# Kernel optimization log

Measured on AMD Instinct MI355X. Metric: run time of the kernel, lower is better.

Reference implementation:

```python
import jax, jax.numpy as jnp
import numpy as np

V, NB, NJ, NP, NK = 6890, 10, 24, 207, 19
PARENTS = np.array([-1, 0, 0, 0, 1, 2, 3, 4, 5, 6, 7, 8, 9, 9, 9, 12, 13, 14, 16, 17, 18, 19, 20, 21])


def setup_inputs():
    key = jax.random.key(0)
    ks = jax.random.split(key, 9)
    B = 1024
    beta = jax.random.normal(ks[0], (B, NB), jnp.float32)
    theta = jax.random.normal(ks[1], (B, NJ * 3), jnp.float32) * 0.3  # axis-angle per joint
    trans = jax.random.normal(ks[2], (B, 3), jnp.float32)
    v_template = jax.random.normal(ks[3], (V, 3), jnp.float32)
    shapedirs = jax.random.normal(ks[4], (NB, V * 3), jnp.float32) * 0.03
    Jr = jax.random.uniform(ks[5], (V, NJ), jnp.float32)
    J_regressor = Jr / jnp.sum(Jr, axis=0, keepdims=True)
    posedirs = jax.random.normal(ks[6], (NP, V * 3), jnp.float32) * 0.01
    jr = jax.random.uniform(ks[7], (V, NK), jnp.float32)
    joint_regressor = jr / jnp.sum(jr, axis=0, keepdims=True)
    w = jax.random.uniform(ks[8], (V, NJ), jnp.float32)
    weights = w / jnp.sum(w, axis=1, keepdims=True)  # LBS weights, rows sum to 1
    return dict(beta=beta, theta=theta, trans=trans, v_template=v_template,
                shapedirs=shapedirs, J_regressor=J_regressor, posedirs=posedirs,
                joint_regressor=joint_regressor, weights=weights)


def batch_rodrigues(theta):
    # theta: (N,3) axis-angle -> (N,3,3) rotation matrices via quaternions (HMR-style)
    angle = jnp.linalg.norm(theta + 1e-8, axis=1, keepdims=True)
    half = angle * 0.5
    v = (theta / angle) * jnp.sin(half)
    quat = jnp.concatenate([jnp.cos(half), v], axis=1)
    quat = quat / jnp.linalg.norm(quat, axis=1, keepdims=True)
    w, x, y, z = quat[:, 0], quat[:, 1], quat[:, 2], quat[:, 3]
    rot = jnp.stack([
        1 - 2 * (y * y + z * z), 2 * (x * y - w * z), 2 * (x * z + w * y),
        2 * (x * y + w * z), 1 - 2 * (x * x + z * z), 2 * (y * z - w * x),
        2 * (x * z - w * y), 2 * (y * z + w * x), 1 - 2 * (x * x + y * y)], axis=1)
    return rot.reshape(-1, 3, 3)


def batch_global_rigid_transformation(Rs, J):
    # Rs: (B,24,3,3), J: (B,24,3); rotate_base=True
    B = Rs.shape[0]
    rot_x = jnp.array([[1., 0., 0.], [0., -1., 0.], [0., 0., -1.]], jnp.float32)
    root_R = Rs[:, 0] @ rot_x

    def make_A(R, t):  # (B,3,3),(B,3) -> (B,4,4)
        top = jnp.concatenate([R, t[:, :, None]], axis=2)
        bot = jnp.broadcast_to(jnp.array([0., 0., 0., 1.], jnp.float32), (B, 1, 4))
        return jnp.concatenate([top, bot], axis=1)

    results = [make_A(root_R, J[:, 0])]
    for i in range(1, NJ):  # fixed 24-joint kinematic chain
        t = J[:, i] - J[:, PARENTS[i]]
        results.append(results[PARENTS[i]] @ make_A(Rs[:, i], t))
    res = jnp.stack(results, axis=1)  # (B,24,4,4)
    new_J = res[:, :, :3, 3]
    j_w0 = jnp.concatenate([J, jnp.zeros_like(J[:, :, :1])], axis=2)  # (B,24,4), homo w=0
    init_bone = jnp.einsum('bjrc,bjc->bjr', res, j_w0)
    A = res.at[:, :, :, 3].add(-init_bone)  # subtract only last column (matches F.pad trick)
    return new_J, A


def reference(beta, theta, trans, v_template, shapedirs, J_regressor, posedirs, joint_regressor, weights):
    B = beta.shape[0]
    v_shaped = (beta @ shapedirs).reshape(B, V, 3) + v_template
    J = jnp.einsum('bvc,vj->bjc', v_shaped, J_regressor)  # (B,24,3)
    Rs = batch_rodrigues(theta.reshape(-1, 3)).reshape(B, NJ, 3, 3)
    pose_feature = (Rs[:, 1:] - jnp.eye(3, dtype=Rs.dtype)).reshape(B, NP)
    v_posed = (pose_feature @ posedirs).reshape(B, V, 3) + v_shaped
    _, A = batch_global_rigid_transformation(Rs, J)
    T = jnp.einsum('vj,bjrc->bvrc', weights, A)  # (B,V,4,4) per-vertex skinning transforms
    homo = jnp.concatenate([v_posed, jnp.ones((B, V, 1), v_posed.dtype)], axis=2)
    verts = jnp.einsum('bvrc,bvc->bvr', T, homo)[:, :, :3] + trans[:, None, :]
    joints = jnp.einsum('bvc,vk->bkc', verts, joint_regressor)  # (B,19,3)
    return joints
```

## Files before the change

kernel.cpp:

```cpp
#include <hip/hip_runtime.h>
#include <hip/hip_bf16.h>

constexpr int Vn   = 6890;
constexpr int VC3  = 20670;
constexpr int NKB  = 216;
constexpr int QT   = 224;
constexpr int NMG  = 14;
constexpr int NCOL = 480;
constexpr int WR   = 1440;
constexpr int MC   = 1368;
constexpr int KSEG = 12;
constexpr int KCH  = 18;
constexpr int RB   = 158;

using bf16x8  = __attribute__((ext_vector_type(8))) short;
using floatx4 = __attribute__((ext_vector_type(4))) float;

__device__ __forceinline__ unsigned short f2bf(float f) {
    unsigned int u = __float_as_uint(f);
    unsigned int r = (u + 0x7FFFu + ((u >> 16) & 1u)) >> 16;
    return (unsigned short)r;
}

__global__ __launch_bounds__(256) void k0_build(
    const float* __restrict__ vt, const float* __restrict__ sdirs,
    const float* __restrict__ pdirs, const float* __restrict__ Jreg,
    const float* __restrict__ jreg, const float* __restrict__ wts,
    unsigned short* __restrict__ Af, unsigned short* __restrict__ Bf,
    float* __restrict__ Jacc)
{
    int bx = blockIdx.x, t = threadIdx.x;
    if (bx < 756) {
        int mg = bx / 54, ub = bx % 54;
        int ql = t & 15, q = mg * 16 + ql;
        int uu = ub * 16 + (t >> 4);
        int v0 = uu * 8, base = 3 * v0;
        float buf[24];
        if (q == 0) {
            #pragma unroll
            for (int i = 0; i < 24; ++i) buf[i] = (v0 + i / 3 < Vn) ? 1.f : 0.f;
        } else {
            const float* src = nullptr;
            if (q == 1) src = vt;
            else if (q >= 2 && q < 12)   src = sdirs + (size_t)(q - 2) * VC3;
            else if (q >= 12 && q < 219) src = pdirs + (size_t)(q - 12) * VC3;
            if (src && base + 23 < VC3) {
                #pragma unroll
                for (int i = 0; i < 12; ++i) {
                    float2 f = *(const float2*)(src + base + 2 * i);
                    buf[2 * i] = f.x; buf[2 * i + 1] = f.y;
                }
            } else {
                #pragma unroll
                for (int i = 0; i < 24; ++i)
                    buf[i] = (src && base + i < VC3) ? src[base + i] : 0.f;
            }
        }
        int kb = uu >> 2, quad = uu & 3;
        size_t foff = (size_t)(ql + quad * 16) * 8;
        #pragma unroll
        for (int c = 0; c < 3; ++c) {
            bf16x8 o;
            #pragma unroll
            for (int j = 0; j < 8; ++j) o[j] = (short)f2bf(buf[3 * j + c]);
            *(bf16x8*)(Af + ((size_t)(c * NMG + mg) * NKB + kb) * 512 + foff) = o;
        }
        return;
    }
    bx -= 756;
    if (bx < 108) {
        int v0 = bx * 64;
        __shared__ float js[64 * 19], wsh[64 * 24], Jsh[64 * 24];
        for (int i = t; i < 64 * 19; i += 256)
            js[i] = (v0 * 19 + i < Vn * 19) ? jreg[v0 * 19 + i] : 0.f;
        for (int i = t; i < 64 * 24; i += 256) {
            wsh[i] = (v0 * 24 + i < Vn * 24) ? wts[v0 * 24 + i] : 0.f;
            Jsh[i] = (v0 * 24 + i < Vn * 24) ? Jreg[v0 * 24 + i] : 0.f;
        }
        __syncthreads();
        for (int s = t; s < 4096; s += 256) {
            int clow = s & 15, w = s >> 4;
            int vg = w & 7, chigh = w >> 3;
            int col = chigh * 16 + clow;
            int kb = (v0 >> 5) + (vg >> 2);
            bf16x8 o;
            #pragma unroll
            for (int j = 0; j < 8; ++j) {
                int vl = vg * 8 + j;
                float val = 0.f;
                if (col < 456)      val = js[vl * 19 + col / 24] * wsh[vl * 24 + col % 24];
                else if (col < 480) val = Jsh[vl * 24 + (col - 456)];
                o[j] = (short)f2bf(val);
            }
            *(bf16x8*)(Bf + ((size_t)chigh * NKB + kb) * 512
                          + (size_t)(clow + (vg & 3) * 16) * 8) = o;
        }
        return;
    }
    for (int i = t; i < 792; i += 256) Jacc[i] = 0.f;
}

__device__ __forceinline__ void k1_load(bf16x8 (&a)[2], bf16x8 (&b)[4],
    const unsigned short* __restrict__ ap, const unsigned short* __restrict__ bp, int i)
{
    a[0] = *(const bf16x8*)(ap + (size_t)(0 * NKB + i) * 512);
    a[1] = *(const bf16x8*)(ap + (size_t)(1 * NKB + i) * 512);
    b[0] = *(const bf16x8*)(bp + (size_t)(0 * NKB + i) * 512);
    b[1] = *(const bf16x8*)(bp + (size_t)(1 * NKB + i) * 512);
    b[2] = *(const bf16x8*)(bp + (size_t)(2 * NKB + i) * 512);
    b[3] = *(const bf16x8*)(bp + (size_t)(3 * NKB + i) * 512);
}

__global__ __launch_bounds__(64) void k1_mfma(
    const unsigned short* __restrict__ Af, const unsigned short* __restrict__ Bf,
    float* __restrict__ P, float* __restrict__ Jacc)
{
    int l = threadIdx.x;
    int bid = blockIdx.x;
    int wid = (bid & 7) * 252 + (bid >> 3);
    int kseg = wid / 168; int r = wid % 168;
    int c = r / 56; r %= 56;
    int mt = r >> 3, nt = r & 7;
    int kb0 = kseg * KCH;

    const unsigned short* ap = Af + ((size_t)(c * NMG + mt * 2) * NKB + kb0) * 512 + l * 8;
    const unsigned short* bp = Bf + ((size_t)(nt * 4) * NKB + kb0) * 512 + l * 8;

    floatx4 acc[2][4];
    #pragma unroll
    for (int mi = 0; mi < 2; ++mi)
        #pragma unroll
        for (int ni = 0; ni < 4; ++ni) acc[mi][ni] = floatx4{0.f, 0.f, 0.f, 0.f};

    bf16x8 a[3][2], b[3][4];
    k1_load(a[0], b[0], ap, bp, 0);
    k1_load(a[1], b[1], ap, bp, 1);
    #pragma unroll
    for (int i = 0; i < KCH; ++i) {
        if (i + 2 < KCH) k1_load(a[(i + 2) % 3], b[(i + 2) % 3], ap, bp, i + 2);
        bf16x8 (&ac)[2] = a[i % 3];
        bf16x8 (&bc)[4] = b[i % 3];
        #pragma unroll
        for (int mi = 0; mi < 2; ++mi)
            #pragma unroll
            for (int ni = 0; ni < 4; ++ni)
                acc[mi][ni] = __builtin_amdgcn_mfma_f32_16x16x32_bf16(ac[mi], bc[ni], acc[mi][ni], 0, 0, 0);
    }
    float* Ps = P + (size_t)kseg * WR * QT;
    int lr = l & 15, rq = (l >> 4) * 4;
    #pragma unroll
    for (int mi = 0; mi < 2; ++mi)
        #pragma unroll
        for (int ni = 0; ni < 4; ++ni) {
            int col = nt * 64 + ni * 16 + lr;
            if (col < NCOL) {
                int q0 = mt * 32 + mi * 16 + rq;
                *(floatx4*)(Ps + (size_t)(col * 3 + c) * QT + q0) = acc[mi][ni];
            }
        }
    if (mt == 0 && nt == 7 && rq < 12) {
        #pragma unroll
        for (int ni = 0; ni < 2; ++ni) {
            int col = 448 + ni * 16 + lr;
            if (col >= 456 && col < 480) {
                #pragma unroll
                for (int rr = 0; rr < 4; ++rr) {
                    int q = rq + rr;
                    if (q >= 1 && q < 12)
                        atomicAdd(&Jacc[(size_t)((col - 456) * 3 + c) * 11 + (q - 1)],
                                  acc[0][ni][rr]);
                }
            }
        }
    }
}

__global__ __launch_bounds__(256) void k12_reduce_prep(
    const float* __restrict__ P, const float* __restrict__ Jacc,
    const float* __restrict__ beta, const float* __restrict__ theta,
    unsigned short* __restrict__ Wb3, float* __restrict__ w1g,
    unsigned short* __restrict__ xbf, float* __restrict__ RAg, float* __restrict__ tAg)
{
    int t = threadIdx.x;
    if (blockIdx.x < RB) {
        int g = blockIdx.x * 256 + t;
        if (g >= WR * 28) return;
        int colc = g / 28, q0 = (g % 28) * 8;
        float v[8] = {0, 0, 0, 0, 0, 0, 0, 0};
        #pragma unroll
        for (int s = 0; s < KSEG; ++s) {
            const float4* p = (const float4*)(P + ((size_t)s * WR + colc) * QT + q0);
            float4 x0 = p[0], x1 = p[1];
            v[0] += x0.x; v[1] += x0.y; v[2] += x0.z; v[3] += x0.w;
            v[4] += x1.x; v[5] += x1.y; v[6] += x1.z; v[7] += x1.w;
        }
        if (colc < 1408) {
            bf16x8 o;
            #pragma unroll
            for (int j = 0; j < 8; ++j)
                o[j] = (short)((colc < MC) ? f2bf(v[j]) : 0);
            *(bf16x8*)(Wb3 + ((size_t)(colc >> 4) * 7 + (q0 >> 5)) * 512
                           + (size_t)((colc & 15) + ((q0 >> 3) & 3) * 16) * 8) = o;
        }
        if (q0 == 0 && colc % 3 == 0 && colc < MC) w1g[colc / 3] = v[0];
        return;
    }
    int b = blockIdx.x - RB;
    __shared__ float Rs[24][9];
    __shared__ float Jl[24][3];
    __shared__ float resR[24][9];
    __shared__ float rest[24][3];
    __shared__ float bet[10];

    if (t < 10) bet[t] = beta[b * 10 + t];
    if (t < 24) {
        float t0 = theta[b * 72 + t * 3 + 0];
        float t1 = theta[b * 72 + t * 3 + 1];
        float t2 = theta[b * 72 + t * 3 + 2];
        float e0 = t0 + 1e-8f, e1 = t1 + 1e-8f, e2 = t2 + 1e-8f;
        float angle = sqrtf(e0 * e0 + e1 * e1 + e2 * e2);
        float half = 0.5f * angle;
        float sh = sinf(half), ch = cosf(half);
        float s = sh / angle;
        float qx = t0 * s, qy = t1 * s, qz = t2 * s;
        float qn = sqrtf(ch * ch + qx * qx + qy * qy + qz * qz);
        float w = ch / qn, x = qx / qn, y = qy / qn, z = qz / qn;
        Rs[t][0] = 1.f - 2.f * (y * y + z * z);
        Rs[t][1] = 2.f * (x * y - w * z);
        Rs[t][2] = 2.f * (x * z + w * y);
        Rs[t][3] = 2.f * (x * y + w * z);
        Rs[t][4] = 1.f - 2.f * (x * x + z * z);
        Rs[t][5] = 2.f * (y * z - w * x);
        Rs[t][6] = 2.f * (x * z - w * y);
        Rs[t][7] = 2.f * (y * z + w * x);
        Rs[t][8] = 1.f - 2.f * (x * x + y * y);
    }
    __syncthreads();
    if (t < 72) {
        const float* basep = Jacc + (size_t)t * 11;
        float acc = basep[0];
        #pragma unroll
        for (int n = 0; n < 10; ++n) acc += bet[n] * basep[1 + n];
        Jl[t / 3][t % 3] = acc;
    }
    for (int q = t; q < QT; q += 256) {
        float xv = 0.f;
        if (q == 1) xv = 1.f;
        else if (q >= 2 && q < 12) xv = bet[q - 2];
        else if (q >= 12 && q < 219) {
            int p = q - 12;
            int jj = 1 + p / 9, e = p % 9;
            float rr = Rs[jj][e];
            if (e == 0 || e == 4 || e == 8) rr -= 1.f;
            xv = rr;
        }
        xbf[((size_t)(b >> 4) * 7 + (q >> 5)) * 512
            + (size_t)((b & 15) + ((q >> 3) & 3) * 16) * 8 + (q & 7)] = f2bf(xv);
    }
    __syncthreads();
    if (t == 0) {
        const int par[24] = {-1,0,0,0,1,2,3,4,5,6,7,8,9,9,9,12,13,14,16,17,18,19,20,21};
        #pragma unroll
        for (int rr = 0; rr < 3; ++rr) {
            resR[0][rr * 3 + 0] =  Rs[0][rr * 3 + 0];
            resR[0][rr * 3 + 1] = -Rs[0][rr * 3 + 1];
            resR[0][rr * 3 + 2] = -Rs[0][rr * 3 + 2];
            rest[0][rr] = Jl[0][rr];
        }
        for (int i = 1; i < 24; ++i) {
            int p = par[i];
            float t0 = Jl[i][0] - Jl[p][0];
            float t1 = Jl[i][1] - Jl[p][1];
            float t2 = Jl[i][2] - Jl[p][2];
            #pragma unroll
            for (int rr = 0; rr < 3; ++rr) {
                float a0 = resR[p][rr * 3 + 0], a1 = resR[p][rr * 3 + 1], a2 = resR[p][rr * 3 + 2];
                resR[i][rr * 3 + 0] = a0 * Rs[i][0] + a1 * Rs[i][3] + a2 * Rs[i][6];
                resR[i][rr * 3 + 1] = a0 * Rs[i][1] + a1 * Rs[i][4] + a2 * Rs[i][7];
                resR[i][rr * 3 + 2] = a0 * Rs[i][2] + a1 * Rs[i][5] + a2 * Rs[i][8];
                rest[i][rr] = a0 * t0 + a1 * t1 + a2 * t2 + rest[p][rr];
            }
        }
    }
    __syncthreads();
    if (t < 216) RAg[(size_t)b * 216 + t] = resR[t / 9][t % 9];
    if (t < 72) {
        int j = t / 3, c = t % 3;
        tAg[(size_t)b * 72 + t] = rest[j][c]
            - (resR[j][c * 3 + 0] * Jl[j][0] + resR[j][c * 3 + 1] * Jl[j][1]
             + resR[j][c * 3 + 2] * Jl[j][2]);
    }
}

__global__ __launch_bounds__(256) void k3_mfma(
    const unsigned short* __restrict__ Wb3, const unsigned short* __restrict__ xbf,
    float* __restrict__ Mg)
{
    int w = threadIdx.x >> 6, l = threadIdx.x & 63;
    int wm = w & 1, wn = w >> 1;
    int ct = blockIdx.x % 22, bt = blockIdx.x / 22;
    int mg0 = ct * 4 + wm * 2;
    int bg0 = bt * 8 + wn * 4;
    const unsigned short* ap = Wb3 + (size_t)mg0 * 7 * 512 + l * 8;
    const unsigned short* bp = xbf + (size_t)bg0 * 7 * 512 + l * 8;

    floatx4 acc[2][4];
    #pragma unroll
    for (int mi = 0; mi < 2; ++mi)
        #pragma unroll
        for (int ni = 0; ni < 4; ++ni) acc[mi][ni] = floatx4{0.f, 0.f, 0.f, 0.f};

    #pragma unroll
    for (int kk = 0; kk < 7; ++kk) {
        bf16x8 a0 = *(const bf16x8*)(ap + (size_t)(0 * 7 + kk) * 512);
        bf16x8 a1 = *(const bf16x8*)(ap + (size_t)(1 * 7 + kk) * 512);
        bf16x8 b0 = *(const bf16x8*)(bp + (size_t)(0 * 7 + kk) * 512);
        bf16x8 b1 = *(const bf16x8*)(bp + (size_t)(1 * 7 + kk) * 512);
        bf16x8 b2 = *(const bf16x8*)(bp + (size_t)(2 * 7 + kk) * 512);
        bf16x8 b3 = *(const bf16x8*)(bp + (size_t)(3 * 7 + kk) * 512);
        acc[0][0] = __builtin_amdgcn_mfma_f32_16x16x32_bf16(a0, b0, acc[0][0], 0, 0, 0);
        acc[0][1] = __builtin_amdgcn_mfma_f32_16x16x32_bf16(a0, b1, acc[0][1], 0, 0, 0);
        acc[0][2] = __builtin_amdgcn_mfma_f32_16x16x32_bf16(a0, b2, acc[0][2], 0, 0, 0);
        acc[0][3] = __builtin_amdgcn_mfma_f32_16x16x32_bf16(a0, b3, acc[0][3], 0, 0, 0);
        acc[1][0] = __builtin_amdgcn_mfma_f32_16x16x32_bf16(a1, b0, acc[1][0], 0, 0, 0);
        acc[1][1] = __builtin_amdgcn_mfma_f32_16x16x32_bf16(a1, b1, acc[1][1], 0, 0, 0);
        acc[1][2] = __builtin_amdgcn_mfma_f32_16x16x32_bf16(a1, b2, acc[1][2], 0, 0, 0);
        acc[1][3] = __builtin_amdgcn_mfma_f32_16x16x32_bf16(a1, b3, acc[1][3], 0, 0, 0);
    }
    int lr = l & 15, rq = (l >> 4) * 4;
    #pragma unroll
    for (int mi = 0; mi < 2; ++mi)
        #pragma unroll
        for (int ni = 0; ni < 4; ++ni) {
            int b  = bt * 128 + wn * 64 + ni * 16 + lr;
            int cc = (mg0 + mi) * 16 + rq;
            if (cc < MC)
                *(floatx4*)(Mg + (size_t)b * MC + cc) = acc[mi][ni];
        }
}

__global__ __launch_bounds__(256) void k4_combine(
    const float* __restrict__ Mg, const float* __restrict__ RAg,
    const float* __restrict__ tAg, const float* __restrict__ w1g,
    const float* __restrict__ trans, float* __restrict__ out)
{
    __shared__ float w1s[456];
    __shared__ float Ms[4 * MC];
    __shared__ float RAs[4 * 216];
    __shared__ float tAs[4 * 72];
    int tid = threadIdx.x;
    int b0 = blockIdx.x * 4;
    for (int i = tid; i < 456; i += 256) w1s[i] = w1g[i];
    for (int i = tid; i < 4 * MC; i += 256) Ms[i] = Mg[(size_t)b0 * MC + i];
    for (int i = tid; i < 4 * 216; i += 256) RAs[i] = RAg[(size_t)b0 * 216 + i];
    for (int i = tid; i < 4 * 72; i += 256) tAs[i] = tAg[(size_t)b0 * 72 + i];
    __syncthreads();
    if (tid < 228) {
        int lb = tid / 57, kc = tid % 57;
        int k = kc / 3, c = kc % 3;
        int b = b0 + lb;
        float acc = trans[b * 3 + c];
        const float* Mrow = Ms + lb * MC;
        const float* RAr  = RAs + lb * 216;
        const float* tAr  = tAs + lb * 72;
        #pragma unroll
        for (int j = 0; j < 24; ++j) {
            int kj = k * 24 + j;
            float m0 = Mrow[kj * 3 + 0], m1 = Mrow[kj * 3 + 1], m2 = Mrow[kj * 3 + 2];
            acc += RAr[j * 9 + c * 3 + 0] * m0
                 + RAr[j * 9 + c * 3 + 1] * m1
                 + RAr[j * 9 + c * 3 + 2] * m2
                 + tAr[j * 3 + c] * w1s[kj];
        }
        out[b * 57 + kc] = acc;
    }
}

extern "C" void kernel_launch(void* const* d_in, const int* in_sizes, int n_in,
                              void* d_out, int out_size, void* d_ws, size_t ws_size,
                              hipStream_t stream)
{
    const float* beta  = (const float*)d_in[0];
    const float* theta = (const float*)d_in[1];
    const float* trans = (const float*)d_in[2];
    const float* vt    = (const float*)d_in[3];
    const float* sdirs = (const float*)d_in[4];
    const float* Jreg  = (const float*)d_in[5];
    const float* pdirs = (const float*)d_in[6];
    const float* jreg  = (const float*)d_in[7];
    const float* wts   = (const float*)d_in[8];
    float* out = (float*)d_out;
    int B = in_sizes[0] / 10;

    unsigned short* Af  = (unsigned short*)d_ws;
    unsigned short* Bf  = Af + (size_t)42 * NKB * 512;
    unsigned short* Wb3 = Bf + (size_t)32 * NKB * 512;
    unsigned short* xbf = Wb3 + (size_t)88 * 7 * 512;
    float* P    = (float*)(xbf + (size_t)64 * 7 * 512);
    float* Jacc = P + (size_t)KSEG * WR * QT;
    float* w1g  = Jacc + 792;
    float* RAg  = w1g + 456;
    float* tAg  = RAg + (size_t)B * 216;
    float* Mg   = tAg + (size_t)B * 72;

    k0_build<<<dim3(756 + 108 + 1), 256, 0, stream>>>(
        vt, sdirs, pdirs, Jreg, jreg, wts, Af, Bf, Jacc);
    k1_mfma<<<dim3(168 * KSEG), 64, 0, stream>>>(Af, Bf, P, Jacc);
    k12_reduce_prep<<<dim3(RB + B), 256, 0, stream>>>(
        P, Jacc, beta, theta, Wb3, w1g, xbf, RAg, tAg);
    k3_mfma<<<dim3((B / 128) * 22), 256, 0, stream>>>(Wb3, xbf, Mg);
    k4_combine<<<dim3(B / 4), 256, 0, stream>>>(Mg, RAg, tAg, w1g, trans, out);
}
```

Before: 141.0 us.

## Replace split-K partials with in-block LDS reduction and fuse per-batch stages

The weight GEMM now runs one 512-thread block per output tile, with eight waves each covering a K segment and reducing through shared memory. The reduced result is written straight to the bf16 Wb3 layout, w1 and Jacc, which removes the large global partial-sum buffer, the separate reduce kernel and the atomics. The per-batch work (Rodrigues, kinematic chain, small GEMM, final combine) is fused into one kernel handling 16 batch items per block, cutting two launches and the RA/tA/xbf round trips. The trade-off is that the first GEMM now runs only 168 blocks, which risks low occupancy. The fused kernel runs its small MFMA GEMM serially per block, and the kinematic chain runs on only 48 threads.

Result: slower. 153.4 us (+8.8%).

```diff
diff --git a/kernel.cpp b/kernel.cpp
--- a/kernel.cpp
+++ b/kernel.cpp
@@ -7,11 +7,8 @@
 constexpr int QT   = 224;
 constexpr int NMG  = 14;
 constexpr int NCOL = 480;
-constexpr int WR   = 1440;
 constexpr int MC   = 1368;
-constexpr int KSEG = 12;
-constexpr int KCH  = 18;
-constexpr int RB   = 158;
+constexpr int KCH  = 27;
 
 using bf16x8  = __attribute__((ext_vector_type(8))) short;
 using floatx4 = __attribute__((ext_vector_type(4))) float;
@@ -26,8 +23,7 @@
     const float* __restrict__ vt, const float* __restrict__ sdirs,
     const float* __restrict__ pdirs, const float* __restrict__ Jreg,
     const float* __restrict__ jreg, const float* __restrict__ wts,
-    unsigned short* __restrict__ Af, unsigned short* __restrict__ Bf,
-    float* __restrict__ Jacc)
+    unsigned short* __restrict__ Af, unsigned short* __restrict__ Bf)
 {
     int bx = blockIdx.x, t = threadIdx.x;
     if (bx < 756) {
@@ -68,7 +64,7 @@
         return;
     }
     bx -= 756;
-    if (bx < 108) {
+    {
         int v0 = bx * 64;
         __shared__ float js[64 * 19], wsh[64 * 24], Jsh[64 * 24];
         for (int i = t; i < 64 * 19; i += 256)
@@ -95,9 +91,7 @@
             *(bf16x8*)(Bf + ((size_t)chigh * NKB + kb) * 512
                           + (size_t)(clow + (vg & 3) * 16) * 8) = o;
         }
-        return;
-    }
-    for (int i = t; i < 792; i += 256) Jacc[i] = 0.f;
+    }
 }
 
 __device__ __forceinline__ void k1_load(bf16x8 (&a)[2], bf16x8 (&b)[4],
@@ -111,17 +105,18 @@
     b[3] = *(const bf16x8*)(bp + (size_t)(3 * NKB + i) * 512);
 }
 
-__global__ __launch_bounds__(64) void k1_mfma(
+__global__ __launch_bounds__(512) void k1_mfma(
     const unsigned short* __restrict__ Af, const unsigned short* __restrict__ Bf,
-    float* __restrict__ P, float* __restrict__ Jacc)
-{
-    int l = threadIdx.x;
-    int bid = blockIdx.x;
-    int wid = (bid & 7) * 252 + (bid >> 3);
-    int kseg = wid / 168; int r = wid % 168;
+    unsigned short* __restrict__ Wb3, float* __restrict__ w1g,
+    float* __restrict__ Jacc)
+{
+    __shared__ float red[8 * 2048];
+    int tid = threadIdx.x;
+    int wv = tid >> 6, l = tid & 63;
+    int r = blockIdx.x;
     int c = r / 56; r %= 56;
     int mt = r >> 3, nt = r & 7;
-    int kb0 = kseg * KCH;
+    int kb0 = wv * KCH;
 
     const unsigned short* ap = Af + ((size_t)(c * NMG + mt * 2) * NKB + kb0) * 512 + l * 8;
     const unsigned short* bp = Bf + ((size_t)(nt * 4) * NKB + kb0) * 512 + l * 8;
@@ -146,77 +141,77 @@
             for (int ni = 0; ni < 4; ++ni)
                 acc[mi][ni] = __builtin_amdgcn_mfma_f32_16x16x32_bf16(ac[mi], bc[ni], acc[mi][ni], 0, 0, 0);
     }
-    float* Ps = P + (size_t)kseg * WR * QT;
-    int lr = l & 15, rq = (l >> 4) * 4;
     #pragma unroll
     for (int mi = 0; mi < 2; ++mi)
         #pragma unroll
-        for (int ni = 0; ni < 4; ++ni) {
-            int col = nt * 64 + ni * 16 + lr;
-            if (col < NCOL) {
-                int q0 = mt * 32 + mi * 16 + rq;
-                *(floatx4*)(Ps + (size_t)(col * 3 + c) * QT + q0) = acc[mi][ni];
+        for (int ni = 0; ni < 4; ++ni)
+            *(floatx4*)&red[wv * 2048 + ((mi * 4 + ni) * 64 + l) * 4] = acc[mi][ni];
+    __syncthreads();
+    if (tid < 256) {
+        int cl = tid & 63, qo = tid >> 6;
+        int ni = cl >> 4;
+        int q0 = qo * 8;
+        int li0 = ((q0 & 15) >> 2) * 16 + (cl & 15);
+        int li1 = (((q0 + 4) & 15) >> 2) * 16 + (cl & 15);
+        int base0 = (((q0 >> 4) * 4 + ni) * 64 + li0) * 4;
+        int base1 = ((((q0 + 4) >> 4) * 4 + ni) * 64 + li1) * 4;
+        floatx4 s0{0.f, 0.f, 0.f, 0.f}, s1{0.f, 0.f, 0.f, 0.f};
+        #pragma unroll
+        for (int ww = 0; ww < 8; ++ww) {
+            s0 += *(const floatx4*)&red[ww * 2048 + base0];
+            s1 += *(const floatx4*)&red[ww * 2048 + base1];
+        }
+        int col = nt * 64 + cl;
+        if (col < NCOL) {
+            int colc = col * 3 + c;
+            if (colc < MC) {
+                bf16x8 o;
+                #pragma unroll
+                for (int j = 0; j < 4; ++j) {
+                    o[j]     = (short)f2bf(s0[j]);
+                    o[4 + j] = (short)f2bf(s1[j]);
+                }
+                *(bf16x8*)(Wb3 + ((size_t)(colc >> 4) * 7 + mt) * 512
+                               + (size_t)((colc & 15) + qo * 16) * 8) = o;
             }
-        }
-    if (mt == 0 && nt == 7 && rq < 12) {
-        #pragma unroll
-        for (int ni = 0; ni < 2; ++ni) {
-            int col = 448 + ni * 16 + lr;
-            if (col >= 456 && col < 480) {
-                #pragma unroll
-                for (int rr = 0; rr < 4; ++rr) {
-                    int q = rq + rr;
-                    if (q >= 1 && q < 12)
-                        atomicAdd(&Jacc[(size_t)((col - 456) * 3 + c) * 11 + (q - 1)],
-                                  acc[0][ni][rr]);
+            if (c == 0 && mt == 0 && qo == 0 && col < 456) w1g[col] = s0[0];
+            if (mt == 0 && col >= 456) {
+                float* jb = Jacc + (size_t)((col - 456) * 3 + c) * 11;
+                if (qo == 0) {
+                    jb[0] = s0[1]; jb[1] = s0[2]; jb[2] = s0[3];
+                    jb[3] = s1[0]; jb[4] = s1[1]; jb[5] = s1[2]; jb[6] = s1[3];
+                } else if (qo == 1) {
+                    jb[7] = s0[0]; jb[8] = s0[1]; jb[9] = s0[2]; jb[10] = s0[3];
                 }
             }
         }
     }
 }
 
-__global__ __launch_bounds__(256) void k12_reduce_prep(
-    const float* __restrict__ P, const float* __restrict__ Jacc,
-    const float* __restrict__ beta, const float* __restrict__ theta,
-    unsigned short* __restrict__ Wb3, float* __restrict__ w1g,
-    unsigned short* __restrict__ xbf, float* __restrict__ RAg, float* __restrict__ tAg)
-{
+__global__ __launch_bounds__(256) void k2_fused(
+    const unsigned short* __restrict__ Wb3, const float* __restrict__ Jacc,
+    const float* __restrict__ w1g, const float* __restrict__ beta,
+    const float* __restrict__ theta, const float* __restrict__ trans,
+    float* __restrict__ Mg, float* __restrict__ out)
+{
+    __shared__ float Rs[16][24][9];
+    __shared__ float Jl[16][24][3];
+    __shared__ float resR[16][24][9];
+    __shared__ float rest_[16][24][3];
+    __shared__ float tA[16][72];
+    __shared__ float bet[16][10];
+    __shared__ float w1s[456];
+    __shared__ unsigned short xls[7 * 512];
     int t = threadIdx.x;
-    if (blockIdx.x < RB) {
-        int g = blockIdx.x * 256 + t;
-        if (g >= WR * 28) return;
-        int colc = g / 28, q0 = (g % 28) * 8;
-        float v[8] = {0, 0, 0, 0, 0, 0, 0, 0};
-        #pragma unroll
-        for (int s = 0; s < KSEG; ++s) {
-            const float4* p = (const float4*)(P + ((size_t)s * WR + colc) * QT + q0);
-            float4 x0 = p[0], x1 = p[1];
-            v[0] += x0.x; v[1] += x0.y; v[2] += x0.z; v[3] += x0.w;
-            v[4] += x1.x; v[5] += x1.y; v[6] += x1.z; v[7] += x1.w;
-        }
-        if (colc < 1408) {
-            bf16x8 o;
-            #pragma unroll
-            for (int j = 0; j < 8; ++j)
-                o[j] = (short)((colc < MC) ? f2bf(v[j]) : 0);
-            *(bf16x8*)(Wb3 + ((size_t)(colc >> 4) * 7 + (q0 >> 5)) * 512
-                           + (size_t)((colc & 15) + ((q0 >> 3) & 3) * 16) * 8) = o;
-        }
-        if (q0 == 0 && colc % 3 == 0 && colc < MC) w1g[colc / 3] = v[0];
-        return;
-    }
-    int b = blockIdx.x - RB;
-    __shared__ float Rs[24][9];
-    __shared__ float Jl[24][3];
-    __shared__ float resR[24][9];
-    __shared__ float rest[24][3];
-    __shared__ float bet[10];
-
-    if (t < 10) bet[t] = beta[b * 10 + t];
-    if (t < 24) {
-        float t0 = theta[b * 72 + t * 3 + 0];
-        float t1 = theta[b * 72 + t * 3 + 1];
-        float t2 = theta[b * 72 + t * 3 + 2];
+    int b0 = blockIdx.x * 16;
+
+    if (t < 160) bet[t / 10][t % 10] = beta[(b0 + t / 10) * 10 + t % 10];
+    for (int i = t; i < 456; i += 256) w1s[i] = w1g[i];
+    for (int i = t; i < 384; i += 256) {
+        int bl = i / 24, j = i % 24;
+        float t0 = theta[(size_t)(b0 + bl) * 72 + j * 3 + 0];
+        float t1 = theta[(size_t)(b0 + bl) * 72 + j * 3 + 1];
+        float t2 = theta[(size_t)(b0 + bl) * 72 + j * 3 + 2];
         float e0 = t0 + 1e-8f, e1 = t1 + 1e-8f, e2 = t2 + 1e-8f;
         float angle = sqrtf(e0 * e0 + e1 * e1 + e2 * e2);
         float half = 0.5f * angle;
@@ -225,152 +220,102 @@
         float qx = t0 * s, qy = t1 * s, qz = t2 * s;
         float qn = sqrtf(ch * ch + qx * qx + qy * qy + qz * qz);
         float w = ch / qn, x = qx / qn, y = qy / qn, z = qz / qn;
-        Rs[t][0] = 1.f - 2.f * (y * y + z * z);
-        Rs[t][1] = 2.f * (x * y - w * z);
-        Rs[t][2] = 2.f * (x * z + w * y);
-        Rs[t][3] = 2.f * (x * y + w * z);
-        Rs[t][4] = 1.f - 2.f * (x * x + z * z);
-        Rs[t][5] = 2.f * (y * z - w * x);
-        Rs[t][6] = 2.f * (x * z - w * y);
-        Rs[t][7] = 2.f * (y * z + w * x);
-        Rs[t][8] = 1.f - 2.f * (x * x + y * y);
-    }
-    __syncthreads();
-    if (t < 72) {
-        const float* basep = Jacc + (size_t)t * 11;
-        float acc = basep[0];
-        #pragma unroll
-        for (int n = 0; n < 10; ++n) acc += bet[n] * basep[1 + n];
-        Jl[t / 3][t % 3] = acc;
-    }
-    for (int q = t; q < QT; q += 256) {
+        Rs[bl][j][0] = 1.f - 2.f * (y * y + z * z);
+        Rs[bl][j][1] = 2.f * (x * y - w * z);
+        Rs[bl][j][2] = 2.f * (x * z + w * y);
+        Rs[bl][j][3] = 2.f * (x * y + w * z);
+        Rs[bl][j][4] = 1.f - 2.f * (x * x + z * z);
+        Rs[bl][j][5] = 2.f * (y * z - w * x);
+        Rs[bl][j][6] = 2.f * (x * z - w * y);
+        Rs[bl][j][7] = 2.f * (y * z + w * x);
+        Rs[bl][j][8] = 1.f - 2.f * (x * x + y * y);
+    }
+    __syncthreads();
+    for (int i = t; i < 16 * 72; i += 256) {
+        int bl = i / 72, jc = i % 72;
+        const float* bp_ = Jacc + (size_t)jc * 11;
+        float a = bp_[0];
+        #pragma unroll
+        for (int n = 0; n < 10; ++n) a += bet[bl][n] * bp_[1 + n];
+        Jl[bl][jc / 3][jc % 3] = a;
+    }
+    for (int i = t; i < 16 * QT; i += 256) {
+        int q = i >> 4, bl = i & 15;
         float xv = 0.f;
         if (q == 1) xv = 1.f;
-        else if (q >= 2 && q < 12) xv = bet[q - 2];
+        else if (q >= 2 && q < 12) xv = bet[bl][q - 2];
         else if (q >= 12 && q < 219) {
             int p = q - 12;
             int jj = 1 + p / 9, e = p % 9;
-            float rr = Rs[jj][e];
+            float rr = Rs[bl][jj][e];
             if (e == 0 || e == 4 || e == 8) rr -= 1.f;
             xv = rr;
         }
-        xbf[((size_t)(b >> 4) * 7 + (q >> 5)) * 512
-            + (size_t)((b & 15) + ((q >> 3) & 3) * 16) * 8 + (q & 7)] = f2bf(xv);
-    }
-    __syncthreads();
-    if (t == 0) {
+        xls[(size_t)(q >> 5) * 512 + (size_t)(bl + ((q >> 3) & 3) * 16) * 8 + (q & 7)]
+            = f2bf(xv);
+    }
+    __syncthreads();
+    {
+        int l = t & 63, wv = t >> 6;
+        bf16x8 xb[7];
+        #pragma unroll
+        for (int kk = 0; kk < 7; ++kk)
+            xb[kk] = *(const bf16x8*)(xls + (size_t)kk * 512 + l * 8);
+        for (int mg = wv; mg < 86; mg += 4) {
+            const unsigned short* apg = Wb3 + (size_t)mg * 7 * 512 + l * 8;
+            floatx4 acc{0.f, 0.f, 0.f, 0.f};
+            #pragma unroll
+            for (int kk = 0; kk < 7; ++kk)
+                acc = __builtin_amdgcn_mfma_f32_16x16x32_bf16(
+                    *(const bf16x8*)(apg + (size_t)kk * 512), xb[kk], acc, 0, 0, 0);
+            int bl = l & 15, cc0 = mg * 16 + (l >> 4) * 4;
+            if (cc0 < MC)
+                *(floatx4*)(Mg + (size_t)(b0 + bl) * MC + cc0) = acc;
+        }
+    }
+    if (t < 48) {
         const int par[24] = {-1,0,0,0,1,2,3,4,5,6,7,8,9,9,9,12,13,14,16,17,18,19,20,21};
-        #pragma unroll
-        for (int rr = 0; rr < 3; ++rr) {
-            resR[0][rr * 3 + 0] =  Rs[0][rr * 3 + 0];
-            resR[0][rr * 3 + 1] = -Rs[0][rr * 3 + 1];
-            resR[0][rr * 3 + 2] = -Rs[0][rr * 3 + 2];
-            rest[0][rr] = Jl[0][rr];
-        }
+        int bl = t / 3, rr = t % 3;
+        resR[bl][0][rr * 3 + 0] =  Rs[bl][0][rr * 3 + 0];
+        resR[bl][0][rr * 3 + 1] = -Rs[bl][0][rr * 3 + 1];
+        resR[bl][0][rr * 3 + 2] = -Rs[bl][0][rr * 3 + 2];
+        rest_[bl][0][rr] = Jl[bl][0][rr];
         for (int i = 1; i < 24; ++i) {
             int p = par[i];
-            float t0 = Jl[i][0] - Jl[p][0];
-            float t1 = Jl[i][1] - Jl[p][1];
-            float t2 = Jl[i][2] - Jl[p][2];
-            #pragma unroll
-            for (int rr = 0; rr < 3; ++rr) {
-                float a0 = resR[p][rr * 3 + 0], a1 = resR[p][rr * 3 + 1], a2 = resR[p][rr * 3 + 2];
-                resR[i][rr * 3 + 0] = a0 * Rs[i][0] + a1 * Rs[i][3] + a2 * Rs[i][6];
-                resR[i][rr * 3 + 1] = a0 * Rs[i][1] + a1 * Rs[i][4] + a2 * Rs[i][7];
-                resR[i][rr * 3 + 2] = a0 * Rs[i][2] + a1 * Rs[i][5] + a2 * Rs[i][8];
-                rest[i][rr] = a0 * t0 + a1 * t1 + a2 * t2 + rest[p][rr];
-            }
-        }
-    }
-    __syncthreads();
-    if (t < 216) RAg[(size_t)b * 216 + t] = resR[t / 9][t % 9];
-    if (t < 72) {
-        int j = t / 3, c = t % 3;
-        tAg[(size_t)b * 72 + t] = rest[j][c]
-            - (resR[j][c * 3 + 0] * Jl[j][0] + resR[j][c * 3 + 1] * Jl[j][1]
-             + resR[j][c * 3 + 2] * Jl[j][2]);
-    }
-}
-
-__global__ __launch_bounds__(256) void k3_mfma(
-    const unsigned short* __restrict__ Wb3, const unsigned short* __restrict__ xbf,
-    float* __restrict__ Mg)
-{
-    int w = threadIdx.x >> 6, l = threadIdx.x & 63;
-    int wm = w & 1, wn = w >> 1;
-    int ct = blockIdx.x % 22, bt = blockIdx.x / 22;
-    int mg0 = ct * 4 + wm * 2;
-    int bg0 = bt * 8 + wn * 4;
-    const unsigned short* ap = Wb3 + (size_t)mg0 * 7 * 512 + l * 8;
-    const unsigned short* bp = xbf + (size_t)bg0 * 7 * 512 + l * 8;
-
-    floatx4 acc[2][4];
-    #pragma unroll
-    for (int mi = 0; mi < 2; ++mi)
-        #pragma unroll
-        for (int ni = 0; ni < 4; ++ni) acc[mi][ni] = floatx4{0.f, 0.f, 0.f, 0.f};
-
-    #pragma unroll
-    for (int kk = 0; kk < 7; ++kk) {
-        bf16x8 a0 = *(const bf16x8*)(ap + (size_t)(0 * 7 + kk) * 512);
-        bf16x8 a1 = *(const bf16x8*)(ap + (size_t)(1 * 7 + kk) * 512);
-        bf16x8 b0 = *(const bf16x8*)(bp + (size_t)(0 * 7 + kk) * 512);
-        bf16x8 b1 = *(const bf16x8*)(bp + (size_t)(1 * 7 + kk) * 512);
-        bf16x8 b2 = *(const bf16x8*)(bp + (size_t)(2 * 7 + kk) * 512);
-        bf16x8 b3 = *(const bf16x8*)(bp + (size_t)(3 * 7 + kk) * 512);
-        acc[0][0] = __builtin_amdgcn_mfma_f32_16x16x32_bf16(a0, b0, acc[0][0], 0, 0, 0);
-        acc[0][1] = __builtin_amdgcn_mfma_f32_16x16x32_bf16(a0, b1, acc[0][1], 0, 0, 0);
-        acc[0][2] = __builtin_amdgcn_mfma_f32_16x16x32_bf16(a0, b2, acc[0][2], 0, 0, 0);
-        acc[0][3] = __builtin_amdgcn_mfma_f32_16x16x32_bf16(a0, b3, acc[0][3], 0, 0, 0);
-        acc[1][0] = __builtin_amdgcn_mfma_f32_16x16x32_bf16(a1, b0, acc[1][0], 0, 0, 0);
-        acc[1][1] = __builtin_amdgcn_mfma_f32_16x16x32_bf16(a1, b1, acc[1][1], 0, 0, 0);
-        acc[1][2] = __builtin_amdgcn_mfma_f32_16x16x32_bf16(a1, b2, acc[1][2], 0, 0, 0);
-        acc[1][3] = __builtin_amdgcn_mfma_f32_16x16x32_bf16(a1, b3, acc[1][3], 0, 0, 0);
-    }
-    int lr = l & 15, rq = (l >> 4) * 4;
-    #pragma unroll
-    for (int mi = 0; mi < 2; ++mi)
-        #pragma unroll
-        for (int ni = 0; ni < 4; ++ni) {
-            int b  = bt * 128 + wn * 64 + ni * 16 + lr;
-            int cc = (mg0 + mi) * 16 + rq;
-            if (cc < MC)
-                *(floatx4*)(Mg + (size_t)b * MC + cc) = acc[mi][ni];
-        }
-}
-
-__global__ __launch_bounds__(256) void k4_combine(
-    const float* __restrict__ Mg, const float* __restrict__ RAg,
-    const float* __restrict__ tAg, const float* __restrict__ w1g,
-    const float* __restrict__ trans, float* __restrict__ out)
-{
-    __shared__ float w1s[456];
-    __shared__ float Ms[4 * MC];
-    __shared__ float RAs[4 * 216];
-    __shared__ float tAs[4 * 72];
-    int tid = threadIdx.x;
-    int b0 = blockIdx.x * 4;
-    for (int i = tid; i < 456; i += 256) w1s[i] = w1g[i];
-    for (int i = tid; i < 4 * MC; i += 256) Ms[i] = Mg[(size_t)b0 * MC + i];
-    for (int i = tid; i < 4 * 216; i += 256) RAs[i] = RAg[(size_t)b0 * 216 + i];
-    for (int i = tid; i < 4 * 72; i += 256) tAs[i] = tAg[(size_t)b0 * 72 + i];
-    __syncthreads();
-    if (tid < 228) {
-        int lb = tid / 57, kc = tid % 57;
+            float t0 = Jl[bl][i][0] - Jl[bl][p][0];
+            float t1 = Jl[bl][i][1] - Jl[bl][p][1];
+            float t2 = Jl[bl][i][2] - Jl[bl][p][2];
+            float a0 = resR[bl][p][rr * 3 + 0], a1 = resR[bl][p][rr * 3 + 1],
+                  a2 = resR[bl][p][rr * 3 + 2];
+            resR[bl][i][rr * 3 + 0] = a0 * Rs[bl][i][0] + a1 * Rs[bl][i][3] + a2 * Rs[bl][i][6];
+            resR[bl][i][rr * 3 + 1] = a0 * Rs[bl][i][1] + a1 * Rs[bl][i][4] + a2 * Rs[bl][i][7];
+            resR[bl][i][rr * 3 + 2] = a0 * Rs[bl][i][2] + a1 * Rs[bl][i][5] + a2 * Rs[bl][i][8];
+            rest_[bl][i][rr] = a0 * t0 + a1 * t1 + a2 * t2 + rest_[bl][p][rr];
+        }
+    }
+    __syncthreads();
+    for (int i = t; i < 16 * 72; i += 256) {
+        int bl = i / 72, jc = i % 72;
+        int j = jc / 3, c = jc % 3;
+        tA[bl][jc] = rest_[bl][j][c]
+            - (resR[bl][j][c * 3 + 0] * Jl[bl][j][0] + resR[bl][j][c * 3 + 1] * Jl[bl][j][1]
+             + resR[bl][j][c * 3 + 2] * Jl[bl][j][2]);
+    }
+    __syncthreads();
+    for (int i = t; i < 16 * 57; i += 256) {
+        int lb = i / 57, kc = i % 57;
         int k = kc / 3, c = kc % 3;
         int b = b0 + lb;
         float acc = trans[b * 3 + c];
-        const float* Mrow = Ms + lb * MC;
-        const float* RAr  = RAs + lb * 216;
-        const float* tAr  = tAs + lb * 72;
+        const float* Mrow = Mg + (size_t)b * MC;
         #pragma unroll
         for (int j = 0; j < 24; ++j) {
             int kj = k * 24 + j;
             float m0 = Mrow[kj * 3 + 0], m1 = Mrow[kj * 3 + 1], m2 = Mrow[kj * 3 + 2];
-            acc += RAr[j * 9 + c * 3 + 0] * m0
-                 + RAr[j * 9 + c * 3 + 1] * m1
-                 + RAr[j * 9 + c * 3 + 2] * m2
-                 + tAr[j * 3 + c] * w1s[kj];
+            acc += resR[lb][j][c * 3 + 0] * m0
+                 + resR[lb][j][c * 3 + 1] * m1
+                 + resR[lb][j][c * 3 + 2] * m2
+                 + tA[lb][j * 3 + c] * w1s[kj];
         }
         out[b * 57 + kc] = acc;
     }
@@ -395,19 +340,13 @@
     unsigned short* Af  = (unsigned short*)d_ws;
     unsigned short* Bf  = Af + (size_t)42 * NKB * 512;
     unsigned short* Wb3 = Bf + (size_t)32 * NKB * 512;
-    unsigned short* xbf = Wb3 + (size_t)88 * 7 * 512;
-    float* P    = (float*)(xbf + (size_t)64 * 7 * 512);
-    float* Jacc = P + (size_t)KSEG * WR * QT;
+    float* Jacc = (float*)(Wb3 + (size_t)88 * 7 * 512);
     float* w1g  = Jacc + 792;
-    float* RAg  = w1g + 456;
-    float* tAg  = RAg + (size_t)B * 216;
-    float* Mg   = tAg + (size_t)B * 72;
-
-    k0_build<<<dim3(756 + 108 + 1), 256, 0, stream>>>(
-        vt, sdirs, pdirs, Jreg, jreg, wts, Af, Bf, Jacc);
-    k1_mfma<<<dim3(168 * KSEG), 64, 0, stream>>>(Af, Bf, P, Jacc);
-    k12_reduce_prep<<<dim3(RB + B), 256, 0, stream>>>(
-        P, Jacc, beta, theta, Wb3, w1g, xbf, RAg, tAg);
-    k3_mfma<<<dim3((B / 128) * 22), 256, 0, stream>>>(Wb3, xbf, Mg);
-    k4_combine<<<dim3(B / 4), 256, 0, stream>>>(Mg, RAg, tAg, w1g, trans, out);
-}
+    float* Mg   = w1g + 456;
+
+    k0_build<<<dim3(756 + 108), 256, 0, stream>>>(
+        vt, sdirs, pdirs, Jreg, jreg, wts, Af, Bf);
+    k1_mfma<<<dim3(168), 512, 0, stream>>>(Af, Bf, Wb3, w1g, Jacc);
+    k2_fused<<<dim3(B / 16), 256, 0, stream>>>(
+        Wb3, Jacc, w1g, beta, theta, trans, Mg, out);
+}
```
